# Performance work log

Hardware: AMD Instinct MI355X
Metric: run time of the kernel (lower is better)

## Reference

```python
import jax, jax.numpy as jnp
import numpy as np

LN_EPS = 1e-5  # torch nn.LayerNorm default eps


def _layernorm(x, g, b):
    m = jnp.mean(x, -1, keepdims=True)
    v = jnp.mean((x - m) ** 2, -1, keepdims=True)
    return (x - m) / jnp.sqrt(v + LN_EPS) * g + b


def _dw_causal_conv(x, w, bias=None):
    # x: (B, L, C); w: (C, K) depthwise kernels; causal via left-pad K-1
    C = x.shape[-1]
    K = w.shape[-1]
    xt = jnp.swapaxes(x, 1, 2)                       # (B, C, L)
    xp = jnp.pad(xt, ((0, 0), (0, 0), (K - 1, 0)))
    y = jax.lax.conv_general_dilated(
        xp, w[:, None, :], (1,), 'VALID',
        feature_group_count=C, dimension_numbers=('NCH', 'OIH', 'NCH'))
    if bias is not None:
        y = y + bias[None, :, None]
    return jnp.swapaxes(y, 1, 2)                     # (B, L, C)


def _s4d(x, Bp, Cp, log_dt, Dp):
    # Diagonal SSM: kernel K[l] = sum_n C[n]*dB[n]*dA[n]^l, shared across channels
    L, Dm = x.shape[1], x.shape[2]
    n = Bp.shape[0]
    A = -jnp.arange(1, n + 1, dtype=x.dtype)
    dt = jnp.clip(jnp.exp(log_dt), 1e-4, 1.0)
    dA = jnp.exp(jnp.clip(dt * A, -10.0, 10.0))                  # (n,)
    dB = (dA - 1.0) / jnp.minimum(A, -1e-4) * Bp                 # (n,)
    pows = dA[:, None] ** jnp.arange(L, dtype=x.dtype)[None, :]  # (n, L)
    Kk = jnp.nan_to_num((Cp * dB) @ pows, nan=0.0, posinf=0.0, neginf=0.0)  # (L,)
    y = _dw_causal_conv(x, jnp.broadcast_to(Kk[None, :], (Dm, L)))
    return y + Dp * x


def _mamba_block(x, g, b, W_in, cw, cb, sB, sC, ldt, sD, W_out, rs):
    res = x
    h = _layernorm(x, g, b)
    xz = h @ W_in.T                                  # (B, L, 2*d_inner)
    xp, z = jnp.split(xz, 2, axis=-1)
    xc = _dw_causal_conv(xp, cw, cb)                 # depthwise causal conv, k=4
    y = _s4d(xc, sB, sC, ldt, sD) * jax.nn.sigmoid(z)
    y = y @ W_out.T
    return res + jnp.clip(rs, 0.0, 1.5) * y          # dropout is identity in eval


def _forward(spatial_tokens_init, pos_embed, ln_g, ln_b, W_in, conv_w, conv_b,
             ssm_B, ssm_C, log_dt, ssm_D, W_out, res_scale, fin_g, fin_b,
             imp_W1, imp_b1, imp_W2, imp_b2, tex_W, tex_b, edge_W, edge_b,
             str_W, str_b):
    x = spatial_tokens_init + pos_embed
    for i in range(ln_g.shape[0]):  # fixed small layer count
        x = _mamba_block(x, ln_g[i], ln_b[i], W_in[i], conv_w[i], conv_b[i],
                         ssm_B[i], ssm_C[i], log_dt[i], ssm_D[i], W_out[i],
                         res_scale[i])
    tokens = _layernorm(x, fin_g, fin_b)
    # F.normalize(dim=-1, eps=1e-6)
    tn = tokens / jnp.maximum(jnp.sqrt(jnp.sum(tokens ** 2, -1, keepdims=True)), 1e-6)
    h = jax.nn.gelu(tn @ imp_W1.T + imp_b1, approximate=False)
    logits = (h @ imp_W2.T + imp_b2)[..., 0]
    w = jax.nn.softmax(logits, axis=-1)
    feats = jnp.sum(tokens * w[..., None], axis=1)
    return (feats,
            feats @ tex_W.T + tex_b,
            feats @ edge_W.T + edge_b,
            feats @ str_W.T + str_b,
            tokens, w)


B, N, D, DI, NL, NS, KC, DH = 512, 256, 128, 256, 4, 16, 4, 64
H = D // 2


def setup_inputs() -> dict:
    ks = jax.random.split(jax.random.key(0), 26)
    r = lambda k, sh, s=0.02: jax.random.normal(k, sh, dtype=jnp.float32) * s
    inp = {
        'spatial_tokens_init': jax.random.normal(ks[0], (B, N, D), dtype=jnp.float32),
        'pos_embed': r(ks[1], (1, N, D)),
        'ln_g': jnp.ones((NL, D), jnp.float32),
        'ln_b': jnp.zeros((NL, D), jnp.float32),
        'W_in': r(ks[2], (NL, 2 * DI, D)),
        'conv_w': r(ks[3], (NL, DI, KC), 0.2),
        'conv_b': r(ks[4], (NL, DI), 0.02),
        'ssm_B': r(ks[5], (NL, NS)),
        'ssm_C': r(ks[6], (NL, NS)),
        'log_dt': jax.random.uniform(ks[7], (NL,), jnp.float32,
                                     minval=float(np.log(1e-3)), maxval=float(np.log(0.1))),
        'ssm_D': jnp.zeros((NL,), jnp.float32),
        'W_out': r(ks[8], (NL, D, DI)),
        'res_scale': jnp.ones((NL,), jnp.float32),
        'fin_g': jnp.ones((D,), jnp.float32),
        'fin_b': jnp.zeros((D,), jnp.float32),
        'imp_W1': r(ks[9], (H, D)),
        'imp_b1': jnp.zeros((H,), jnp.float32),
        'imp_W2': r(ks[10], (1, H)),
        'imp_b2': jnp.zeros((1,), jnp.float32),
        'tex_W': r(ks[11], (DH, D)),
        'tex_b': jnp.zeros((DH,), jnp.float32),
        'edge_W': r(ks[12], (DH, D)),
        'edge_b': jnp.zeros((DH,), jnp.float32),
        'str_W': r(ks[13], (DH, D)),
        'str_b': jnp.zeros((DH,), jnp.float32),
    }
    return inp


def reference(spatial_tokens_init, pos_embed, ln_g, ln_b, W_in, conv_w, conv_b,
              ssm_B, ssm_C, log_dt, ssm_D, W_out, res_scale, fin_g, fin_b,
              imp_W1, imp_b1, imp_W2, imp_b2, tex_W, tex_b, edge_W, edge_b,
              str_W, str_b):
    return _forward(spatial_tokens_init, pos_embed, ln_g, ln_b, W_in, conv_w,
                    conv_b, ssm_B, ssm_C, log_dt, ssm_D, W_out, res_scale,
                    fin_g, fin_b, imp_W1, imp_b1, imp_W2, imp_b2, tex_W, tex_b,
                    edge_W, edge_b, str_W, str_b)
```

## Files before the change

### kernel.cpp

```cpp
#include <hip/hip_runtime.h>
#include <hip/hip_bf16.h>


typedef __bf16 bf16_8 __attribute__((ext_vector_type(8)));
typedef __bf16 bf16_4 __attribute__((ext_vector_type(4)));
typedef float  f32_4  __attribute__((ext_vector_type(4)));

#define GLOAD16(src, dst) __builtin_amdgcn_global_load_lds( \
    (const __attribute__((address_space(1))) void*)(src),   \
    (__attribute__((address_space(3))) void*)(dst), 16, 0, 0)

__device__ __forceinline__ float fsig(float z) {
    float e = __expf(-z);
    return __builtin_amdgcn_rcpf(1.0f + e);
}

__global__ __launch_bounds__(256) void prep_kernel(const float* __restrict__ win,
                                                   const float* __restrict__ wout,
                                                   const float* __restrict__ w1,
                                                   __bf16* __restrict__ win16,
                                                   __bf16* __restrict__ wout16,
                                                   __bf16* __restrict__ w116) {
    int i = blockIdx.x * 256 + threadIdx.x;
    if (i < 4 * 512 * 128) win16[i] = (__bf16)win[i];
    if (i < 4 * 128 * 256) wout16[i] = (__bf16)wout[i];
    if (i < 64 * 128)      w116[i]  = (__bf16)w1[i];
}

__global__ __launch_bounds__(256) void build_T_kernel(const float* __restrict__ Bp,
                                                      const float* __restrict__ Cp,
                                                      const float* __restrict__ ldt,
                                                      const float* __restrict__ Dpv,
                                                      __bf16* __restrict__ Tg,
                                                      float* __restrict__ Rg) {
    __shared__ float rsum[4];
    int layer = blockIdx.y, l = blockIdx.x, j = threadIdx.x;
    int d = l - j;
    float val = 0.0f;
    if (d >= 0) {
        float dt = expf(ldt[layer]);
        dt = fminf(fmaxf(dt, 1e-4f), 1.0f);
        #pragma unroll
        for (int n = 0; n < 16; ++n) {
            float A = -(float)(n + 1);
            float e = fminf(fmaxf(dt * A, -10.0f), 10.0f);
            float dA = expf(e);
            float dB = (dA - 1.0f) / A * Bp[layer * 16 + n];
            val += Cp[layer * 16 + n] * dB * expf(e * (float)d);
        }
        if (d == 0) val += Dpv[layer];
    }
    __bf16 bv = (__bf16)val;
    Tg[layer * 65536 + l * 256 + j] = bv;
    float fv = (float)bv;
    #pragma unroll
    for (int o = 32; o; o >>= 1) fv += __shfl_xor(fv, o);
    int lane = j & 63, wave = j >> 6;
    if (lane == 0) rsum[wave] = fv;
    __syncthreads();
    if (j == 0) Rg[layer * 256 + l] = rsum[0] + rsum[1] + rsum[2] + rsum[3];
}

__global__ __launch_bounds__(256) void ln_first_kernel(const float4* __restrict__ init4,
                                                       const float4* __restrict__ pos4,
                                                       const float* __restrict__ g,
                                                       const float* __restrict__ bta,
                                                       __bf16* __restrict__ x,
                                                       __bf16* __restrict__ h) {
    int tid = threadIdx.x;
    int wave = tid >> 6, lane = tid & 63;
    int half = lane >> 5, l32 = lane & 31;
    long tok = (long)blockIdx.x * 8 + wave * 2 + half;
    float4 v = init4[tok * 32 + l32];
    float4 p = pos4[(tok & 255) * 32 + l32];
    v.x += p.x; v.y += p.y; v.z += p.z; v.w += p.w;
    int d0 = l32 * 4;
    bf16_4 xv;
    xv[0] = (__bf16)v.x; xv[1] = (__bf16)v.y; xv[2] = (__bf16)v.z; xv[3] = (__bf16)v.w;
    *(bf16_4*)(x + tok * 128 + d0) = xv;
    float s = v.x + v.y + v.z + v.w;
    float ss = v.x * v.x + v.y * v.y + v.z * v.z + v.w * v.w;
    #pragma unroll
    for (int o = 16; o; o >>= 1) { s += __shfl_xor(s, o); ss += __shfl_xor(ss, o); }
    float m = s * (1.0f / 128.0f);
    float var = ss * (1.0f / 128.0f) - m * m;
    float r = rsqrtf(var + 1e-5f);
    bf16_4 hv;
    hv[0] = (__bf16)((v.x - m) * r * g[d0]     + bta[d0]);
    hv[1] = (__bf16)((v.y - m) * r * g[d0 + 1] + bta[d0 + 1]);
    hv[2] = (__bf16)((v.z - m) * r * g[d0 + 2] + bta[d0 + 2]);
    hv[3] = (__bf16)((v.w - m) * r * g[d0 + 3] + bta[d0 + 3]);
    *(bf16_4*)(h + tok * 128 + d0) = hv;
}

__global__ __launch_bounds__(256) void gemm1_kernel(const __bf16* __restrict__ hmat,
                                                    const __bf16* __restrict__ win,
                                                    __bf16* __restrict__ xpt) {
    __shared__ __align__(16) __bf16 As[128 * 64];
    __shared__ __align__(16) __bf16 Bs[128 * 64];
    int tid = threadIdx.x;
    int bid = blockIdx.x;
    long m0 = (long)((bid & 7) + ((bid >> 4) << 3)) * 128;
    int n0 = ((bid >> 3) & 1) * 128;
    int wave = tid >> 6, lane = tid & 63;
    int wm = wave >> 1, wn = wave & 1;
    int lrow = lane & 15, lk = (lane >> 4) * 8;
    int r7 = lrow & 7;
    int rl = lane >> 3, sl = lane & 7;
    int scol = ((sl ^ rl) << 3);
    f32_4 acc[4][4] = {};

    for (int kc = 0; kc < 2; ++kc) {
        const __bf16* asrc = hmat + m0 * 128 + kc * 64;
        const __bf16* bsrc = win + (long)n0 * 128 + kc * 64;
        #pragma unroll
        for (int j = 0; j < 4; ++j) {
            int chunk = wave * 4 + j;
            GLOAD16(asrc + (long)(chunk * 8 + rl) * 128 + scol, As + chunk * 512);
            GLOAD16(bsrc + (long)(chunk * 8 + rl) * 128 + scol, Bs + chunk * 512);
        }
        __syncthreads();
        #pragma unroll
        for (int kk = 0; kk < 64; kk += 32) {
            int sw = ((((kk + lk) >> 3) ^ r7) << 3);
            bf16_8 a[4], b[4];
            #pragma unroll
            for (int mt = 0; mt < 4; ++mt)
                a[mt] = *(const bf16_8*)(As + (wm * 64 + mt * 16 + lrow) * 64 + sw);
            #pragma unroll
            for (int nt = 0; nt < 4; ++nt)
                b[nt] = *(const bf16_8*)(Bs + (wn * 64 + nt * 16 + lrow) * 64 + sw);
            #pragma unroll
            for (int mt = 0; mt < 4; ++mt)
                #pragma unroll
                for (int nt = 0; nt < 4; ++nt)
                    acc[mt][nt] = __builtin_amdgcn_mfma_f32_16x16x32_bf16(
                        a[mt], b[nt], acc[mt][nt], 0, 0, 0);
        }
        __syncthreads();
    }

    int row_base = (lane >> 4) * 4;
    int col = lane & 15;
    #pragma unroll
    for (int mt = 0; mt < 4; ++mt) {
        long mg = m0 + wm * 64 + mt * 16 + row_base;
        int b = (int)(mg >> 8), l = (int)(mg & 255);
        #pragma unroll
        for (int nt = 0; nt < 4; ++nt) {
            int ng = n0 + wn * 64 + nt * 16 + col;
            bf16_4 o;
            #pragma unroll
            for (int r = 0; r < 4; ++r) o[r] = (__bf16)acc[mt][nt][r];
            *(bf16_4*)(xpt + (long)b * 65536 + (long)ng * 256 + l) = o;
        }
    }
}

__global__ __launch_bounds__(512) void ssm_gemm_kernel(const __bf16* __restrict__ xct,
                                                       const __bf16* __restrict__ hmat,
                                                       const __bf16* __restrict__ winz,
                                                       __bf16* __restrict__ yb,
                                                       const __bf16* __restrict__ Tg,
                                                       const float* __restrict__ Rg,
                                                       const float* __restrict__ cw,
                                                       const float* __restrict__ cb) {
    __shared__ __align__(16) __bf16 As[256 * 64];
    __shared__ __align__(16) __bf16 Bs[128 * 64];
    __shared__ float  bnd[3][128];
    __shared__ float  Rs[256];
    int tid = threadIdx.x;
    int batch = blockIdx.x >> 1;
    int ntile = blockIdx.x & 1;
    int c0 = ntile * 128;

    int wave = tid >> 6, lane = tid & 63;
    int wm = wave >> 2, wn = wave & 3;
    int lrow = lane & 15, lk = (lane >> 4) * 8;
    int r7 = lrow & 7;
    int quad = lane >> 4;
    int rl = lane >> 3, sl = lane & 7;
    int scol = ((sl ^ rl) << 3);
    f32_4 acc[8][2] = {};
    f32_4 accz[8][2] = {};

    if (tid < 256) Rs[tid] = Rg[tid];

    const __bf16* hsrc0 = hmat + (long)batch * 32768;
    for (int kc = 0; kc < 2; ++kc) {
        int j0 = kc * 64;
        #pragma unroll
        for (int j = 0; j < 4; ++j) {
            int chunk = wave * 4 + j;
            GLOAD16(hsrc0 + (long)(chunk * 8 + rl) * 128 + j0 + scol, As + chunk * 512);
        }
        #pragma unroll
        for (int j = 0; j < 2; ++j) {
            int chunk = wave * 2 + j;
            GLOAD16(winz + (long)(c0 + chunk * 8 + rl) * 128 + j0 + scol, Bs + chunk * 512);
        }
        __syncthreads();
        #pragma unroll
        for (int kk = 0; kk < 64; kk += 32) {
            int sw = ((((kk + lk) >> 3) ^ r7) << 3);
            bf16_8 b0 = *(const bf16_8*)(Bs + (wn * 32 + lrow) * 64 + sw);
            bf16_8 b1 = *(const bf16_8*)(Bs + (wn * 32 + 16 + lrow) * 64 + sw);
            #pragma unroll
            for (int mt = 0; mt < 8; ++mt) {
                bf16_8 a = *(const bf16_8*)(As + (wm * 128 + mt * 16 + lrow) * 64 + sw);
                accz[mt][0] = __builtin_amdgcn_mfma_f32_16x16x32_bf16(a, b0, accz[mt][0], 0, 0, 0);
                accz[mt][1] = __builtin_amdgcn_mfma_f32_16x16x32_bf16(a, b1, accz[mt][1], 0, 0, 0);
            }
        }
        __syncthreads();
    }

    const __bf16* bsrc0 = xct + (long)batch * 65536 + (long)c0 * 256;
    for (int kc = 0; kc < 4; ++kc) {
        int j0 = kc * 64;
        const __bf16* asrc = Tg + j0;
        const __bf16* bsrc = bsrc0 + j0;
        #pragma unroll
        for (int j = 0; j < 4; ++j) {
            int chunk = wave * 4 + j;
            GLOAD16(asrc + (long)(chunk * 8 + rl) * 256 + scol, As + chunk * 512);
        }
        #pragma unroll
        for (int j = 0; j < 2; ++j) {
            int chunk = wave * 2 + j;
            GLOAD16(bsrc + (long)(chunk * 8 + rl) * 256 + scol, Bs + chunk * 512);
        }
        __syncthreads();
        #pragma unroll
        for (int kk = 0; kk < 64; kk += 32) {
            int sw = ((((kk + lk) >> 3) ^ r7) << 3);
            bf16_8 b0 = *(const bf16_8*)(Bs + (wn * 32 + lrow) * 64 + sw);
            bf16_8 b1 = *(const bf16_8*)(Bs + (wn * 32 + 16 + lrow) * 64 + sw);
            #pragma unroll
            for (int mt = 0; mt < 8; ++mt) {
                bf16_8 a = *(const bf16_8*)(As + (wm * 128 + mt * 16 + lrow) * 64 + sw);
                acc[mt][0] = __builtin_amdgcn_mfma_f32_16x16x32_bf16(a, b0, acc[mt][0], 0, 0, 0);
                acc[mt][1] = __builtin_amdgcn_mfma_f32_16x16x32_bf16(a, b1, acc[mt][1], 0, 0, 0);
            }
        }
        __syncthreads();
    }

    if (wm == 0 && quad == 3) {
        #pragma unroll
        for (int nt = 0; nt < 2; ++nt) {
            int colb = wn * 32 + nt * 16 + lrow;
            bnd[0][colb] = acc[7][nt][1];
            bnd[1][colb] = acc[7][nt][2];
            bnd[2][colb] = acc[7][nt][3];
        }
    }
    __syncthreads();

    float4 wv[2]; float cbv[2];
    #pragma unroll
    for (int nt = 0; nt < 2; ++nt) {
        int cg = c0 + wn * 32 + nt * 16 + lrow;
        wv[nt] = *(const float4*)(cw + cg * 4);
        cbv[nt] = cb[cg];
    }
    int src = (lane + 48) & 63;

    #pragma unroll
    for (int mt = 0; mt < 8; ++mt) {
        int lbase = wm * 128 + mt * 16 + quad * 4;
        int mp = mt > 0 ? mt - 1 : 0;
        float R0 = Rs[lbase], R1 = Rs[lbase + 1], R2 = Rs[lbase + 2], R3 = Rs[lbase + 3];
        #pragma unroll
        for (int nt = 0; nt < 2; ++nt) {
            int colb = wn * 32 + nt * 16 + lrow;
            int cg = c0 + colb;
            float s1 = __shfl(acc[mt][nt][3], src);
            float s2 = __shfl(acc[mt][nt][2], src);
            float s3 = __shfl(acc[mt][nt][1], src);
            float t1, t2, t3;
            if (mt == 0) {
                if (wm == 1) { t1 = bnd[2][colb]; t2 = bnd[1][colb]; t3 = bnd[0][colb]; }
                else         { t1 = 0.0f; t2 = 0.0f; t3 = 0.0f; }
            } else {
                t1 = __shfl(acc[mp][nt][3], src);
                t2 = __shfl(acc[mp][nt][2], src);
                t3 = __shfl(acc[mp][nt][1], src);
            }
            float pm1 = quad ? s1 : t1;
            float pm2 = quad ? s2 : t2;
            float pm3 = quad ? s3 : t3;
            float p0 = acc[mt][nt][0], p1 = acc[mt][nt][1];
            float p2 = acc[mt][nt][2], p3 = acc[mt][nt][3];
            float y0 = wv[nt].x * pm3 + wv[nt].y * pm2 + wv[nt].z * pm1 + wv[nt].w * p0 + cbv[nt] * R0;
            float y1 = wv[nt].x * pm2 + wv[nt].y * pm1 + wv[nt].z * p0  + wv[nt].w * p1 + cbv[nt] * R1;
            float y2 = wv[nt].x * pm1 + wv[nt].y * p0  + wv[nt].z * p1  + wv[nt].w * p2 + cbv[nt] * R2;
            float y3 = wv[nt].x * p0  + wv[nt].y * p1  + wv[nt].z * p2  + wv[nt].w * p3 + cbv[nt] * R3;
            long base = (long)batch * 65536 + (long)lbase * 256 + cg;
            yb[base]       = (__bf16)(y0 * fsig(accz[mt][nt][0]));
            yb[base + 256] = (__bf16)(y1 * fsig(accz[mt][nt][1]));
            yb[base + 512] = (__bf16)(y2 * fsig(accz[mt][nt][2]));
            yb[base + 768] = (__bf16)(y3 * fsig(accz[mt][nt][3]));
        }
    }
}

__global__ __launch_bounds__(256) void gemm2_kernel(const __bf16* __restrict__ y,
                                                    const __bf16* __restrict__ wout,
                                                    __bf16* __restrict__ x,
                                                    const float* __restrict__ rs_p,
                                                    const float* __restrict__ g,
                                                    const float* __restrict__ bta,
                                                    __bf16* __restrict__ hout,
                                                    float* __restrict__ tokens_out,
                                                    int final_mode) {
    __shared__ __align__(16) __bf16 As[64 * 64];
    __shared__ __align__(16) __bf16 Bs[128 * 64];
    __shared__ float s_sum[64][2];
    __shared__ float s_ssq[64][2];
    int tid = threadIdx.x;
    long m0 = (long)blockIdx.x * 64;
    int wave = tid >> 6, lane = tid & 63;
    int wm = wave >> 1, wn = wave & 1;
    int lrow = lane & 15, lk = (lane >> 4) * 8;
    int r7 = lrow & 7;
    int rl = lane >> 3, sl = lane & 7;
    int scol = ((sl ^ rl) << 3);
    f32_4 acc[2][4] = {};

    for (int kc = 0; kc < 4; ++kc) {
        const __bf16* asrc = y + m0 * 256 + kc * 64;
        const __bf16* bsrc = wout + kc * 64;
        #pragma unroll
        for (int j = 0; j < 2; ++j) {
            int chunk = wave * 2 + j;
            GLOAD16(asrc + (long)(chunk * 8 + rl) * 256 + scol, As + chunk * 512);
        }
        #pragma unroll
        for (int j = 0; j < 4; ++j) {
            int chunk = wave * 4 + j;
            GLOAD16(bsrc + (long)(chunk * 8 + rl) * 256 + scol, Bs + chunk * 512);
        }
        __syncthreads();
        #pragma unroll
        for (int kk = 0; kk < 64; kk += 32) {
            int sw = ((((kk + lk) >> 3) ^ r7) << 3);
            bf16_8 a[2], b[4];
            #pragma unroll
            for (int mt = 0; mt < 2; ++mt)
                a[mt] = *(const bf16_8*)(As + (wm * 32 + mt * 16 + lrow) * 64 + sw);
            #pragma unroll
            for (int nt = 0; nt < 4; ++nt)
                b[nt] = *(const bf16_8*)(Bs + (wn * 64 + nt * 16 + lrow) * 64 + sw);
            #pragma unroll
            for (int mt = 0; mt < 2; ++mt)
                #pragma unroll
                for (int nt = 0; nt < 4; ++nt)
                    acc[mt][nt] = __builtin_amdgcn_mfma_f32_16x16x32_bf16(
                        a[mt], b[nt], acc[mt][nt], 0, 0, 0);
        }
        __syncthreads();
    }

    float rs = rs_p[0];
    rs = fminf(fmaxf(rs, 0.0f), 1.5f);
    int quad = lane >> 4;
    int col = lane & 15;

    #pragma unroll
    for (int mt = 0; mt < 2; ++mt) {
        int tb = wm * 32 + mt * 16 + quad * 4;
        long mg = m0 + tb;
        #pragma unroll
        for (int r = 0; r < 4; ++r) {
            float s = 0.0f, ss = 0.0f;
            #pragma unroll
            for (int nt = 0; nt < 4; ++nt) {
                int d = wn * 64 + nt * 16 + col;
                float xv = (float)x[(mg + r) * 128 + d] + rs * acc[mt][nt][r];
                acc[mt][nt][r] = xv;
                s += xv; ss += xv * xv;
            }
            #pragma unroll
            for (int o = 8; o; o >>= 1) { s += __shfl_xor(s, o); ss += __shfl_xor(ss, o); }
            if (col == 0) {
                s_sum[tb + r][wn] = s;
                s_ssq[tb + r][wn] = ss;
            }
        }
    }
    __syncthreads();

    #pragma unroll
    for (int mt = 0; mt < 2; ++mt) {
        int tb = wm * 32 + mt * 16 + quad * 4;
        long mg = m0 + tb;
        #pragma unroll
        for (int r = 0; r < 4; ++r) {
            float s  = s_sum[tb + r][0] + s_sum[tb + r][1];
            float ss = s_ssq[tb + r][0] + s_ssq[tb + r][1];
            float m = s * (1.0f / 128.0f);
            float var = ss * (1.0f / 128.0f) - m * m;
            float rstd = rsqrtf(var + 1e-5f);
            #pragma unroll
            for (int nt = 0; nt < 4; ++nt) {
                int d = wn * 64 + nt * 16 + col;
                float xv = acc[mt][nt][r];
                float t = (xv - m) * rstd * g[d] + bta[d];
                if (!final_mode) {
                    x[(mg + r) * 128 + d] = (__bf16)xv;
                    hout[(mg + r) * 128 + d] = (__bf16)t;
                } else {
                    tokens_out[(mg + r) * 128 + d] = t;
                }
            }
        }
    }
}

__global__ __launch_bounds__(256) void l2n_kernel(const float4* __restrict__ tokens4,
                                                  __bf16* __restrict__ tn) {
    int tid = threadIdx.x;
    int wave = tid >> 6, lane = tid & 63;
    int half = lane >> 5, l32 = lane & 31;
    long tok = (long)blockIdx.x * 8 + wave * 2 + half;
    float4 t = tokens4[tok * 32 + l32];
    float q = t.x * t.x + t.y * t.y + t.z * t.z + t.w * t.w;
    #pragma unroll
    for (int o = 16; o; o >>= 1) q += __shfl_xor(q, o);
    float inv = 1.0f / fmaxf(sqrtf(q), 1e-6f);
    bf16_4 o4;
    o4[0] = (__bf16)(t.x * inv); o4[1] = (__bf16)(t.y * inv);
    o4[2] = (__bf16)(t.z * inv); o4[3] = (__bf16)(t.w * inv);
    *(bf16_4*)(tn + tok * 128 + l32 * 4) = o4;
}

#define LDA 136
__global__ __launch_bounds__(256) void mlp_kernel(const __bf16* __restrict__ tn,
                                                  const __bf16* __restrict__ w1b,
                                                  const float* __restrict__ b1,
                                                  const float* __restrict__ W2,
                                                  const float* __restrict__ b2,
                                                  float* __restrict__ logits) {
    __shared__ __bf16 As[128 * LDA];
    __shared__ __bf16 Bs[64 * LDA];
    int tid = threadIdx.x;
    long m0 = (long)blockIdx.x * 128;
    const __bf16* asrc = tn + m0 * 128;
    #pragma unroll
    for (int i = 0; i < 8; ++i) {
        int idx = tid + i * 256;
        int row = idx >> 4, c = idx & 15;
        uint4 v = *(const uint4*)(asrc + row * 128 + c * 8);
        *(uint4*)(As + row * LDA + c * 8) = v;
    }
    #pragma unroll
    for (int i = 0; i < 4; ++i) {
        int idx = tid + i * 256;
        int row = idx >> 4, c = idx & 15;
        uint4 v = *(const uint4*)(w1b + row * 128 + c * 8);
        *(uint4*)(Bs + row * LDA + c * 8) = v;
    }
    __syncthreads();

    int wave = tid >> 6, lane = tid & 63;
    int lrow = lane & 15, lk = (lane >> 4) * 8;
    f32_4 acc[2][4] = {};
    #pragma unroll
    for (int kk = 0; kk < 128; kk += 32) {
        bf16_8 a[2], b[4];
        #pragma unroll
        for (int mt = 0; mt < 2; ++mt)
            a[mt] = *(const bf16_8*)(As + (wave * 32 + mt * 16 + lrow) * LDA + kk + lk);
        #pragma unroll
        for (int nt = 0; nt < 4; ++nt)
            b[nt] = *(const bf16_8*)(Bs + (nt * 16 + lrow) * LDA + kk + lk);
        #pragma unroll
        for (int mt = 0; mt < 2; ++mt)
            #pragma unroll
            for (int nt = 0; nt < 4; ++nt)
                acc[mt][nt] = __builtin_amdgcn_mfma_f32_16x16x32_bf16(
                    a[mt], b[nt], acc[mt][nt], 0, 0, 0);
    }

    int col = lane & 15, quad = lane >> 4;
    float b2v = b2[0];
    #pragma unroll
    for (int mt = 0; mt < 2; ++mt) {
        #pragma unroll
        for (int r = 0; r < 4; ++r) {
            float p = 0.0f;
            #pragma unroll
            for (int nt = 0; nt < 4; ++nt) {
                int jx = nt * 16 + col;
                float a = acc[mt][nt][r] + b1[jx];
                float gl = 0.5f * a * (1.0f + erff(a * 0.70710678118654752f));
                p += gl * W2[jx];
            }
            #pragma unroll
            for (int o = 8; o; o >>= 1) p += __shfl_xor(p, o);
            if (col == 0) {
                long tok = m0 + wave * 32 + mt * 16 + quad * 4 + r;
                logits[tok] = p + b2v;
            }
        }
    }
}

__global__ __launch_bounds__(256) void head_kernel(const float* __restrict__ tokens,
                                                   const float* __restrict__ logits,
                                                   const float* __restrict__ texW,
                                                   const float* __restrict__ texb,
                                                   const float* __restrict__ edgeW,
                                                   const float* __restrict__ edgeb,
                                                   const float* __restrict__ strW,
                                                   const float* __restrict__ strb,
                                                   float* __restrict__ feats_out,
                                                   float* __restrict__ tex_out,
                                                   float* __restrict__ edge_out,
                                                   float* __restrict__ str_out,
                                                   float* __restrict__ w_out) {
    __shared__ float wsm[256];
    __shared__ float red[8];
    __shared__ float feats_s[128];
    int b = blockIdx.x, tid = threadIdx.x;
    int lane = tid & 63, wave = tid >> 6;
    float lg = logits[(long)b * 256 + tid];
    float mx = lg;
    #pragma unroll
    for (int o = 32; o; o >>= 1) mx = fmaxf(mx, __shfl_xor(mx, o));
    if (lane == 0) red[wave] = mx;
    __syncthreads();
    float bm = fmaxf(fmaxf(red[0], red[1]), fmaxf(red[2], red[3]));
    float e = expf(lg - bm);
    float se = e;
    #pragma unroll
    for (int o = 32; o; o >>= 1) se += __shfl_xor(se, o);
    if (lane == 0) red[4 + wave] = se;
    __syncthreads();
    float tot = red[4] + red[5] + red[6] + red[7];
    float w = e / tot;
    wsm[tid] = w;
    w_out[(long)b * 256 + tid] = w;
    __syncthreads();
    if (tid < 128) {
        float acc = 0.0f;
        const float* tb = tokens + (long)b * 256 * 128 + tid;
        #pragma unroll 4
        for (int l = 0; l < 256; ++l) acc += tb[l * 128] * wsm[l];
        feats_s[tid] = acc;
        feats_out[(long)b * 128 + tid] = acc;
    }
    __syncthreads();
    if (tid < 192) {
        int head = tid >> 6, j = tid & 63;
        const float* W  = head == 0 ? texW : (head == 1 ? edgeW : strW);
        const float* bi = head == 0 ? texb : (head == 1 ? edgeb : strb);
        float* outp     = head == 0 ? tex_out : (head == 1 ? edge_out : str_out);
        const float* wr = W + j * 128;
        float acc = 0.0f;
        #pragma unroll 8
        for (int k = 0; k < 128; ++k) acc += feats_s[k] * wr[k];
        outp[(long)b * 64 + j] = acc + bi[j];
    }
}

extern "C" void kernel_launch(void* const* d_in, const int* in_sizes, int n_in,
                              void* d_out, int out_size, void* d_ws, size_t ws_size,
                              hipStream_t stream) {
    const float* init   = (const float*)d_in[0];
    const float* pos    = (const float*)d_in[1];
    const float* ln_g   = (const float*)d_in[2];
    const float* ln_b   = (const float*)d_in[3];
    const float* W_in   = (const float*)d_in[4];
    const float* conv_w = (const float*)d_in[5];
    const float* conv_b = (const float*)d_in[6];
    const float* ssm_B  = (const float*)d_in[7];
    const float* ssm_C  = (const float*)d_in[8];
    const float* log_dt = (const float*)d_in[9];
    const float* ssm_D  = (const float*)d_in[10];
    const float* W_out  = (const float*)d_in[11];
    const float* res_sc = (const float*)d_in[12];
    const float* fin_g  = (const float*)d_in[13];
    const float* fin_b  = (const float*)d_in[14];
    const float* imp_W1 = (const float*)d_in[15];
    const float* imp_b1 = (const float*)d_in[16];
    const float* imp_W2 = (const float*)d_in[17];
    const float* imp_b2 = (const float*)d_in[18];
    const float* tex_W  = (const float*)d_in[19];
    const float* tex_b  = (const float*)d_in[20];
    const float* edge_W = (const float*)d_in[21];
    const float* edge_b = (const float*)d_in[22];
    const float* str_W  = (const float*)d_in[23];
    const float* str_b  = (const float*)d_in[24];

    float* out = (float*)d_out;
    char* ws = (char*)d_ws;
    __bf16* x      = (__bf16*)ws;
    __bf16* xpt    = (__bf16*)(ws + 67108864);
    __bf16* yb     = (__bf16*)(ws + 134217728);
    __bf16* hb     = (__bf16*)(ws + 201326592);
    __bf16* win16  = (__bf16*)(ws + 234881024);
    __bf16* wout16 = (__bf16*)(ws + 235405312);
    float*  logits = (float*)(ws + 235667456);
    __bf16* w1b    = (__bf16*)(ws + 236191744);
    __bf16* Tg     = (__bf16*)(ws + 236208128);
    float*  Rg     = (float*)(ws + 236732416);

    float* tokens = out + 163840;

    prep_kernel<<<1024, 256, 0, stream>>>(W_in, W_out, imp_W1, win16, wout16, w1b);
    build_T_kernel<<<dim3(256, 4), 256, 0, stream>>>(ssm_B, ssm_C, log_dt, ssm_D, Tg, Rg);
    ln_first_kernel<<<16384, 256, 0, stream>>>((const float4*)init, (const float4*)pos,
                                               ln_g, ln_b, x, hb);
    for (int l = 0; l < 4; ++l) {
        gemm1_kernel<<<2048, 256, 0, stream>>>(hb, win16 + l * 65536, xpt);
        ssm_gemm_kernel<<<1024, 512, 0, stream>>>(xpt, hb, win16 + l * 65536 + 32768,
                                                  yb, Tg + l * 65536, Rg + l * 256,
                                                  conv_w + l * 1024, conv_b + l * 256);
        int fin = (l == 3);
        const float* gn = fin ? fin_g : ln_g + (l + 1) * 128;
        const float* bn = fin ? fin_b : ln_b + (l + 1) * 128;
        gemm2_kernel<<<2048, 256, 0, stream>>>(yb, wout16 + l * 32768, x, res_sc + l,
                                               gn, bn, hb, fin ? tokens : nullptr, fin);
    }
    __bf16* tn = hb;
    l2n_kernel<<<16384, 256, 0, stream>>>((const float4*)tokens, tn);
    mlp_kernel<<<1024, 256, 0, stream>>>(tn, w1b, imp_b1, imp_W2, imp_b2, logits);
    head_kernel<<<512, 256, 0, stream>>>(tokens, logits, tex_W, tex_b, edge_W, edge_b,
                                         str_W, str_b, out, out + 65536, out + 98304,
                                         out + 131072, out + 16941056);
}
```

Baseline: 699.6 us.

## Double-buffer LDS tiles with async prefetch in SSM and output GEMM kernels

Both the SSM GEMM kernel and the output-projection GEMM kernel now use two LDS buffers. The next K-chunk is loaded asynchronously with global_load_lds while the current chunk runs through MFMA, and explicit vmcnt waits plus raw barriers replace __syncthreads. The SSM kernel also merges its two K loops into one twelve-stage pipeline with 32-wide chunks and a new XOR swizzle. This is meant to hide global-memory latency behind compute. In exchange it uses more LDS per block in gemm2, which may lower occupancy, and it relies on hand-counted vmcnt values being correct.

```diff
diff --git a/kernel.cpp b/kernel.cpp
--- a/kernel.cpp
+++ b/kernel.cpp
@@ -9,6 +9,11 @@
 #define GLOAD16(src, dst) __builtin_amdgcn_global_load_lds( \
     (const __attribute__((address_space(1))) void*)(src),   \
     (__attribute__((address_space(3))) void*)(dst), 16, 0, 0)
+
+#define VMCNT(N) asm volatile("s_waitcnt vmcnt(" #N ")" ::: "memory")
+#define RBAR() do { asm volatile("" ::: "memory"); \
+                    __builtin_amdgcn_s_barrier();  \
+                    asm volatile("" ::: "memory"); } while (0)
 
 __device__ __forceinline__ float fsig(float z) {
     float e = __expf(-z);
@@ -165,8 +170,8 @@
                                                        const float* __restrict__ Rg,
                                                        const float* __restrict__ cw,
                                                        const float* __restrict__ cb) {
-    __shared__ __align__(16) __bf16 As[256 * 64];
-    __shared__ __align__(16) __bf16 Bs[128 * 64];
+    __shared__ __align__(16) __bf16 As[2][256 * 32];
+    __shared__ __align__(16) __bf16 Bs[2][128 * 32];
     __shared__ float  bnd[3][128];
     __shared__ float  Rs[256];
     int tid = threadIdx.x;
@@ -176,74 +181,58 @@
 
     int wave = tid >> 6, lane = tid & 63;
     int wm = wave >> 2, wn = wave & 3;
-    int lrow = lane & 15, lk = (lane >> 4) * 8;
-    int r7 = lrow & 7;
+    int lrow = lane & 15;
     int quad = lane >> 4;
-    int rl = lane >> 3, sl = lane & 7;
-    int scol = ((sl ^ rl) << 3);
     f32_4 acc[8][2] = {};
     f32_4 accz[8][2] = {};
 
     if (tid < 256) Rs[tid] = Rg[tid];
 
-    const __bf16* hsrc0 = hmat + (long)batch * 32768;
-    for (int kc = 0; kc < 2; ++kc) {
-        int j0 = kc * 64;
-        #pragma unroll
-        for (int j = 0; j < 4; ++j) {
-            int chunk = wave * 4 + j;
-            GLOAD16(hsrc0 + (long)(chunk * 8 + rl) * 128 + j0 + scol, As + chunk * 512);
-        }
-        #pragma unroll
-        for (int j = 0; j < 2; ++j) {
-            int chunk = wave * 2 + j;
-            GLOAD16(winz + (long)(c0 + chunk * 8 + rl) * 128 + j0 + scol, Bs + chunk * 512);
-        }
-        __syncthreads();
-        #pragma unroll
-        for (int kk = 0; kk < 64; kk += 32) {
-            int sw = ((((kk + lk) >> 3) ^ r7) << 3);
-            bf16_8 b0 = *(const bf16_8*)(Bs + (wn * 32 + lrow) * 64 + sw);
-            bf16_8 b1 = *(const bf16_8*)(Bs + (wn * 32 + 16 + lrow) * 64 + sw);
-            #pragma unroll
-            for (int mt = 0; mt < 8; ++mt) {
-                bf16_8 a = *(const bf16_8*)(As + (wm * 128 + mt * 16 + lrow) * 64 + sw);
-                accz[mt][0] = __builtin_amdgcn_mfma_f32_16x16x32_bf16(a, b0, accz[mt][0], 0, 0, 0);
-                accz[mt][1] = __builtin_amdgcn_mfma_f32_16x16x32_bf16(a, b1, accz[mt][1], 0, 0, 0);
-            }
-        }
-        __syncthreads();
-    }
-
-    const __bf16* bsrc0 = xct + (long)batch * 65536 + (long)c0 * 256;
-    for (int kc = 0; kc < 4; ++kc) {
-        int j0 = kc * 64;
-        const __bf16* asrc = Tg + j0;
-        const __bf16* bsrc = bsrc0 + j0;
-        #pragma unroll
-        for (int j = 0; j < 4; ++j) {
-            int chunk = wave * 4 + j;
-            GLOAD16(asrc + (long)(chunk * 8 + rl) * 256 + scol, As + chunk * 512);
-        }
-        #pragma unroll
-        for (int j = 0; j < 2; ++j) {
-            int chunk = wave * 2 + j;
-            GLOAD16(bsrc + (long)(chunk * 8 + rl) * 256 + scol, Bs + chunk * 512);
-        }
-        __syncthreads();
-        #pragma unroll
-        for (int kk = 0; kk < 64; kk += 32) {
-            int sw = ((((kk + lk) >> 3) ^ r7) << 3);
-            bf16_8 b0 = *(const bf16_8*)(Bs + (wn * 32 + lrow) * 64 + sw);
-            bf16_8 b1 = *(const bf16_8*)(Bs + (wn * 32 + 16 + lrow) * 64 + sw);
-            #pragma unroll
-            for (int mt = 0; mt < 8; ++mt) {
-                bf16_8 a = *(const bf16_8*)(As + (wm * 128 + mt * 16 + lrow) * 64 + sw);
-                acc[mt][0] = __builtin_amdgcn_mfma_f32_16x16x32_bf16(a, b0, acc[mt][0], 0, 0, 0);
-                acc[mt][1] = __builtin_amdgcn_mfma_f32_16x16x32_bf16(a, b1, acc[mt][1], 0, 0, 0);
-            }
-        }
-        __syncthreads();
+    const __bf16* hsrc  = hmat + (long)batch * 32768;
+    const __bf16* wzsrc = winz + (long)c0 * 128;
+    const __bf16* xsrc  = xct + (long)batch * 65536 + (long)c0 * 256;
+
+    auto STAGE = [&](int c, int b) {
+        const __bf16 *aS, *bS; long astr, bstr;
+        if (c < 4) { int j0 = c * 32;       aS = hsrc + j0; astr = 128; bS = wzsrc + j0; bstr = 128; }
+        else       { int j0 = (c - 4) * 32; aS = Tg + j0;   astr = 256; bS = xsrc + j0;  bstr = 256; }
+        __bf16* Ab = As[b]; __bf16* Bb = Bs[b];
+        #pragma unroll
+        for (int rnd = 0; rnd < 2; ++rnd) {
+            int idx = tid + rnd * 512;
+            int r = idx >> 2, u = idx & 3;
+            GLOAD16(aS + (long)r * astr + ((u ^ ((r >> 1) & 3)) << 3), Ab + idx * 8);
+        }
+        {
+            int r = tid >> 2, u = tid & 3;
+            GLOAD16(bS + (long)r * bstr + ((u ^ ((r >> 1) & 3)) << 3), Bb + tid * 8);
+        }
+    };
+    auto CHUNK = [&](int b, f32_4 (*dst)[2]) {
+        const __bf16* Ab = As[b]; const __bf16* Bb = Bs[b];
+        int rb0 = wn * 32 + lrow, rb1 = rb0 + 16;
+        bf16_8 b0 = *(const bf16_8*)(Bb + rb0 * 32 + ((quad ^ ((rb0 >> 1) & 3)) << 3));
+        bf16_8 b1 = *(const bf16_8*)(Bb + rb1 * 32 + ((quad ^ ((rb1 >> 1) & 3)) << 3));
+        #pragma unroll
+        for (int mt = 0; mt < 8; ++mt) {
+            int ra = wm * 128 + mt * 16 + lrow;
+            bf16_8 a = *(const bf16_8*)(Ab + ra * 32 + ((quad ^ ((ra >> 1) & 3)) << 3));
+            dst[mt][0] = __builtin_amdgcn_mfma_f32_16x16x32_bf16(a, b0, dst[mt][0], 0, 0, 0);
+            dst[mt][1] = __builtin_amdgcn_mfma_f32_16x16x32_bf16(a, b1, dst[mt][1], 0, 0, 0);
+        }
+    };
+
+    STAGE(0, 0);
+    VMCNT(0);
+    RBAR();
+    for (int t = 0; t < 12; ++t) {
+        int cur = t & 1;
+        if (t < 11) { STAGE(t + 1, cur ^ 1); VMCNT(3); }
+        else        { VMCNT(0); }
+        RBAR();
+        if (t < 4) CHUNK(cur, accz);
+        else       CHUNK(cur, acc);
+        RBAR();
     }
 
     if (wm == 0 && quad == 3) {
@@ -314,8 +303,8 @@
                                                     __bf16* __restrict__ hout,
                                                     float* __restrict__ tokens_out,
                                                     int final_mode) {
-    __shared__ __align__(16) __bf16 As[64 * 64];
-    __shared__ __align__(16) __bf16 Bs[128 * 64];
+    __shared__ __align__(16) __bf16 As[2][64 * 64];
+    __shared__ __align__(16) __bf16 Bs[2][128 * 64];
     __shared__ float s_sum[64][2];
     __shared__ float s_ssq[64][2];
     int tid = threadIdx.x;
@@ -328,30 +317,39 @@
     int scol = ((sl ^ rl) << 3);
     f32_4 acc[2][4] = {};
 
-    for (int kc = 0; kc < 4; ++kc) {
+    auto STAGE = [&](int kc, int b) {
         const __bf16* asrc = y + m0 * 256 + kc * 64;
         const __bf16* bsrc = wout + kc * 64;
         #pragma unroll
         for (int j = 0; j < 2; ++j) {
             int chunk = wave * 2 + j;
-            GLOAD16(asrc + (long)(chunk * 8 + rl) * 256 + scol, As + chunk * 512);
+            GLOAD16(asrc + (long)(chunk * 8 + rl) * 256 + scol, As[b] + chunk * 512);
         }
         #pragma unroll
         for (int j = 0; j < 4; ++j) {
             int chunk = wave * 4 + j;
-            GLOAD16(bsrc + (long)(chunk * 8 + rl) * 256 + scol, Bs + chunk * 512);
-        }
-        __syncthreads();
+            GLOAD16(bsrc + (long)(chunk * 8 + rl) * 256 + scol, Bs[b] + chunk * 512);
+        }
+    };
+
+    STAGE(0, 0);
+    VMCNT(0);
+    RBAR();
+    for (int kc = 0; kc < 4; ++kc) {
+        int cur = kc & 1;
+        if (kc < 3) { STAGE(kc + 1, cur ^ 1); VMCNT(6); }
+        else        { VMCNT(0); }
+        RBAR();
         #pragma unroll
         for (int kk = 0; kk < 64; kk += 32) {
             int sw = ((((kk + lk) >> 3) ^ r7) << 3);
             bf16_8 a[2], b[4];
             #pragma unroll
             for (int mt = 0; mt < 2; ++mt)
-                a[mt] = *(const bf16_8*)(As + (wm * 32 + mt * 16 + lrow) * 64 + sw);
+                a[mt] = *(const bf16_8*)(As[cur] + (wm * 32 + mt * 16 + lrow) * 64 + sw);
             #pragma unroll
             for (int nt = 0; nt < 4; ++nt)
-                b[nt] = *(const bf16_8*)(Bs + (wn * 64 + nt * 16 + lrow) * 64 + sw);
+                b[nt] = *(const bf16_8*)(Bs[cur] + (wn * 64 + nt * 16 + lrow) * 64 + sw);
             #pragma unroll
             for (int mt = 0; mt < 2; ++mt)
                 #pragma unroll
@@ -359,7 +357,7 @@
                     acc[mt][nt] = __builtin_amdgcn_mfma_f32_16x16x32_bf16(
                         a[mt], b[nt], acc[mt][nt], 0, 0, 0);
         }
-        __syncthreads();
+        RBAR();
     }
 
     float rs = rs_p[0];
```

Measured after the change: 766.2 us. 9.5% more time.
